# Kernel optimization log

Hardware: AMD Instinct MI355X
Metric: run time of the kernel (lower is better)

The kernel has to match this reference:

```python
import jax, jax.numpy as jnp
import numpy as np

SHIFT = 1  # shift_direction fixed to +1 (module draws +/-1 at random)


def setup_inputs() -> dict:
    key = jax.random.key(0)
    k1, k2 = jax.random.split(key)
    x = jax.random.normal(k1, (128, 48, 28, 28), dtype=jnp.float32)
    w = jax.random.normal(k2, (24, 96, 7), dtype=jnp.float32)  # (Cin, Cout, K) per group, shared across groups
    return {"x": x, "w": w}


def reference(x, w):
    B, H, W = 128, 28, 28
    G, CIN, COUT, K = 2, 24, 96, 7
    # x -> (B, G, Cin, H, W); the unfold/einsum is a grouped conv1d over W (axis 'm'),
    # with H (axis 'n') untouched -> fold H into the batch dim.
    x5 = x.reshape(B, G, CIN, H, W)
    xc = x5.transpose(0, 3, 1, 2, 4).reshape(B * H, G * CIN, W)  # (B*H, 48, W)
    # kernel (Cout, Cin, K); same weights for both groups -> tile to (G*Cout, Cin, K)
    kern = jnp.tile(jnp.transpose(w, (1, 0, 2)), (G, 1, 1))  # (192, 24, 7)
    y = jax.lax.conv_general_dilated(
        xc, kern, window_strides=(1,), padding=[(3, 3)],
        dimension_numbers=('NCH', 'OIH', 'NCH'), feature_group_count=G)  # (B*H, 192, W)
    y = y.reshape(B, H, G * COUT, W).transpose(0, 2, 1, 3)  # (B, 192, H, W), channels group-major = (o, i)
    return jnp.roll(y, SHIFT, axis=2)  # roll along H (original dim 2)
```

## Files before the change

kernel.cpp:

```cpp
#include <hip/hip_runtime.h>


typedef __attribute__((ext_vector_type(8))) short short8;
typedef __attribute__((ext_vector_type(4))) float float4v;

#define B_     128
#define H_     28
#define W_     28
#define CIN_   24
#define COUT_  96
#define K_     7
#define KSTEPS 6
#define NT_    6
#define MT_    7
#define HW_    784

static __device__ __forceinline__ short f2bf(float f) {
    union { float f; unsigned u; } v; v.f = f;
    return (short)((v.u + 0x7fffu + ((v.u >> 16) & 1u)) >> 16);
}

static __device__ __forceinline__ unsigned cvt_pk_bf16(float a, float b) {
    unsigned r;
    asm("v_cvt_pk_bf16_f32 %0, %1, %2" : "=v"(r) : "v"(a), "v"(b));
    return r;
}

__global__ __launch_bounds__(64)
void wfrag_kernel(const float* __restrict__ w, short8* __restrict__ wf) {
    const int idx  = blockIdx.x;
    const int ks   = idx / 6, nt = idx - ks * 6;
    const int lane = threadIdx.x;
    const int c    = nt * 16 + (lane & 15);
    const int q    = ks * 4 + (lane >> 4);
    short8 v;
    if (q < 21) {
        const int k   = (q * 11) >> 5;
        const int ci0 = (q - 3 * k) * 8;
#pragma unroll
        for (int j = 0; j < 8; ++j)
            v[j] = f2bf(w[(ci0 + j) * (COUT_ * K_) + c * K_ + k]);
    } else {
#pragma unroll
        for (int j = 0; j < 8; ++j) v[j] = 0;
    }
    wf[idx * 64 + lane] = v;
}

__global__ __launch_bounds__(384, 6)
void conv_mfma_kernel(const float* __restrict__ x,
                      const short8* __restrict__ wfg,
                      float* __restrict__ out) {
    const int bid = blockIdx.x;
    const int ht  = bid % 7;
    const int bg  = bid / 7;
    const int g   = bg & 1;
    const int b   = bg >> 1;
    const int tid  = threadIdx.x;
    const int lane = tid & 63;
    const int nt   = tid >> 6;
    const int cgrp = lane & 15;
    const int kgrp = lane >> 4;

    __shared__ __align__(16) short xs[4 * 36 * 24];

    float v0r[5], v1r[5];
#pragma unroll
    for (int it = 0; it < 5; ++it) {
        const int idx = tid + it * 384;
        if (idx < 1728) {
            const int p  = idx % 36;
            const int r  = idx / 36;
            const int cp = r % 12;
            const int hl = r / 12;
            const int ws = p - 3;
            const int rsrc = (4 * ht + hl + 27) % 28;
            float a0 = 0.0f, a1 = 0.0f;
            if (ws >= 0 && ws < W_) {
                const size_t base =
                    ((size_t)(b * 48 + g * CIN_ + cp * 2) * H_ + rsrc) * W_ + ws;
                a0 = x[base];
                a1 = x[base + (size_t)HW_];
            }
            v0r[it] = a0; v1r[it] = a1;
        }
    }

    short8 br[KSTEPS];
#pragma unroll
    for (int ks = 0; ks < KSTEPS; ++ks)
        br[ks] = wfg[(ks * NT_ + nt) * 64 + lane];

#pragma unroll
    for (int it = 0; it < 5; ++it) {
        const int idx = tid + it * 384;
        if (idx < 1728) {
            const int p  = idx % 36;
            const int r  = idx / 36;
            const int cp = r % 12;
            const int hl = r / 12;
            ((unsigned*)xs)[(hl * 36 + p) * 12 + cp] = cvt_pk_bf16(v0r[it], v1r[it]);
        }
    }
    __syncthreads();

    int koff[KSTEPS];
#pragma unroll
    for (int ks = 0; ks < KSTEPS; ++ks) {
        const int q   = ks * 4 + kgrp;
        const int k   = (q * 11) >> 5;
        const int ci0 = (q - 3 * k) * 8;
        koff[ks] = k * 24 + ci0;
    }

    const int c_out = nt * 16 + cgrp;
    float* cbase = out + ((size_t)(b * 192 + g * COUT_ + c_out)) * HW_;

#pragma unroll
    for (int mt = 0; mt < MT_; ++mt) {
        const int mA = mt * 16 + cgrp;
        const int hA = mA / 28;
        const int tA = mA - hA * 28;
        const int abase = (hA * 36 + tA) * 24;
        float4v acc = (float4v)(0.0f);
#pragma unroll
        for (int ks = 0; ks < KSTEPS; ++ks) {
            const short8 a = *(const short8*)&xs[abase + koff[ks]];
            acc = __builtin_amdgcn_mfma_f32_16x16x32_bf16(a, br[ks], acc, 0, 0, 0);
        }
        const int m0 = mt * 16 + kgrp * 4;
        const int hl = m0 / 28;
        const int t0 = m0 - hl * 28;
        const int hd = 4 * ht + hl;
        float4 v; v.x = acc[0]; v.y = acc[1]; v.z = acc[2]; v.w = acc[3];
        *(float4*)&cbase[hd * W_ + t0] = v;
    }
}

extern "C" void kernel_launch(void* const* d_in, const int* in_sizes, int n_in,
                              void* d_out, int out_size, void* d_ws, size_t ws_size,
                              hipStream_t stream) {
    const float* x = (const float*)d_in[0];
    const float* w = (const float*)d_in[1];
    float* out = (float*)d_out;
    short8* wf = (short8*)d_ws;

    wfrag_kernel<<<36, 64, 0, stream>>>(w, wf);
    conv_mfma_kernel<<<B_ * 2 * 7, 384, 0, stream>>>(x, wf, out);
}
```

Baseline: 28.24 us.

## Split waves over M and N-pairs to reuse A fragments; pad LDS rows

Each wave now computes two 16-column output tiles (N-pair) for half of the M tiles instead of one N tile for all seven M tiles, so every LDS A-fragment load feeds two MFMAs. The LDS row stride is padded from 24 to 26 shorts to reduce bank conflicts on the fragment reads. In exchange each wave holds twice the B fragments and two accumulators, raising register pressure, so launch bounds drop occupancy from 6 to 4. The M split is also uneven (4 tiles versus 3), which leaves some waves idle at the end.

```diff
diff --git a/kernel.cpp b/kernel.cpp
--- a/kernel.cpp
+++ b/kernel.cpp
@@ -12,8 +12,8 @@
 #define K_     7
 #define KSTEPS 6
 #define NT_    6
-#define MT_    7
 #define HW_    784
+#define XROW   26
 
 static __device__ __forceinline__ short f2bf(float f) {
     union { float f; unsigned u; } v; v.f = f;
@@ -47,7 +47,7 @@
     wf[idx * 64 + lane] = v;
 }
 
-__global__ __launch_bounds__(384, 6)
+__global__ __launch_bounds__(384, 4)
 void conv_mfma_kernel(const float* __restrict__ x,
                       const short8* __restrict__ wfg,
                       float* __restrict__ out) {
@@ -58,11 +58,13 @@
     const int b   = bg >> 1;
     const int tid  = threadIdx.x;
     const int lane = tid & 63;
-    const int nt   = tid >> 6;
+    const int wv   = tid >> 6;
+    const int np   = wv >> 1;
+    const int mh   = wv & 1;
     const int cgrp = lane & 15;
     const int kgrp = lane >> 4;
 
-    __shared__ __align__(16) short xs[4 * 36 * 24];
+    __shared__ __align__(16) short xs[4 * 36 * XROW];
 
     float v0r[5], v1r[5];
 #pragma unroll
@@ -86,10 +88,12 @@
         }
     }
 
-    short8 br[KSTEPS];
+    short8 br0[KSTEPS], br1[KSTEPS];
 #pragma unroll
-    for (int ks = 0; ks < KSTEPS; ++ks)
-        br[ks] = wfg[(ks * NT_ + nt) * 64 + lane];
+    for (int ks = 0; ks < KSTEPS; ++ks) {
+        br0[ks] = wfg[(ks * NT_ + 2 * np)     * 64 + lane];
+        br1[ks] = wfg[(ks * NT_ + 2 * np + 1) * 64 + lane];
+    }
 
 #pragma unroll
     for (int it = 0; it < 5; ++it) {
@@ -99,7 +103,7 @@
             const int r  = idx / 36;
             const int cp = r % 12;
             const int hl = r / 12;
-            ((unsigned*)xs)[(hl * 36 + p) * 12 + cp] = cvt_pk_bf16(v0r[it], v1r[it]);
+            ((unsigned*)xs)[(hl * 36 + p) * 13 + cp] = cvt_pk_bf16(v0r[it], v1r[it]);
         }
     }
     __syncthreads();
@@ -110,30 +114,42 @@
         const int q   = ks * 4 + kgrp;
         const int k   = (q * 11) >> 5;
         const int ci0 = (q - 3 * k) * 8;
-        koff[ks] = k * 24 + ci0;
+        koff[ks] = k * XROW + ci0;
     }
 
-    const int c_out = nt * 16 + cgrp;
-    float* cbase = out + ((size_t)(b * 192 + g * COUT_ + c_out)) * HW_;
+    const int c_out0 = (2 * np)     * 16 + cgrp;
+    const int c_out1 = (2 * np + 1) * 16 + cgrp;
+    float* cb0 = out + ((size_t)(b * 192 + g * COUT_ + c_out0)) * HW_;
+    float* cb1 = out + ((size_t)(b * 192 + g * COUT_ + c_out1)) * HW_;
+
+    const int mt0 = mh * 4;
+    const int mtn = mh ? 3 : 4;
 
 #pragma unroll
-    for (int mt = 0; mt < MT_; ++mt) {
-        const int mA = mt * 16 + cgrp;
-        const int hA = mA / 28;
-        const int tA = mA - hA * 28;
-        const int abase = (hA * 36 + tA) * 24;
-        float4v acc = (float4v)(0.0f);
+    for (int mti = 0; mti < 4; ++mti) {
+        if (mti < mtn) {
+            const int mt = mt0 + mti;
+            const int mA = mt * 16 + cgrp;
+            const int hA = mA / 28;
+            const int tA = mA - hA * 28;
+            const int abase = (hA * 36 + tA) * XROW;
+            float4v a0 = (float4v)(0.0f);
+            float4v a1 = (float4v)(0.0f);
 #pragma unroll
-        for (int ks = 0; ks < KSTEPS; ++ks) {
-            const short8 a = *(const short8*)&xs[abase + koff[ks]];
-            acc = __builtin_amdgcn_mfma_f32_16x16x32_bf16(a, br[ks], acc, 0, 0, 0);
+            for (int ks = 0; ks < KSTEPS; ++ks) {
+                const short8 a = *(const short8*)&xs[abase + koff[ks]];
+                a0 = __builtin_amdgcn_mfma_f32_16x16x32_bf16(a, br0[ks], a0, 0, 0, 0);
+                a1 = __builtin_amdgcn_mfma_f32_16x16x32_bf16(a, br1[ks], a1, 0, 0, 0);
+            }
+            const int m0 = mt * 16 + kgrp * 4;
+            const int hl = m0 / 28;
+            const int t0 = m0 - hl * 28;
+            const int hd = 4 * ht + hl;
+            float4 u0; u0.x = a0[0]; u0.y = a0[1]; u0.z = a0[2]; u0.w = a0[3];
+            float4 u1; u1.x = a1[0]; u1.y = a1[1]; u1.z = a1[2]; u1.w = a1[3];
+            *(float4*)&cb0[hd * W_ + t0] = u0;
+            *(float4*)&cb1[hd * W_ + t0] = u1;
         }
-        const int m0 = mt * 16 + kgrp * 4;
-        const int hl = m0 / 28;
-        const int t0 = m0 - hl * 28;
-        const int hd = 4 * ht + hl;
-        float4 v; v.x = acc[0]; v.y = acc[1]; v.z = acc[2]; v.w = acc[3];
-        *(float4*)&cbase[hd * W_ + t0] = v;
     }
 }
 
```

Measured after the change: 33.27 us. 17.8% more time.

## Pre-transpose input to padded bf16 layout and stream tiles via global_load_lds

Applied to the files above, without the earlier changes.

Adds a separate pass that converts x to a padded, rolled, channel-pair-packed bf16 buffer in workspace, with the weight-fragment build folded into that same pass. The conv kernel then copies its contiguous slice straight into LDS with global_load_lds, which removes the per-thread strided gather, the conversion and the register staging. In exchange the whole input is written to and read back from global memory in an extra kernel. The old path is kept as a fallback when the workspace is too small.

```diff
diff --git a/kernel.cpp b/kernel.cpp
--- a/kernel.cpp
+++ b/kernel.cpp
@@ -14,25 +14,32 @@
 #define NT_    6
 #define MT_    7
 #define HW_    784
+#define WFBYTES   36864
+#define XBFDWORDS 3096576
+#define XBFBYTES  (XBFDWORDS * 4)
 
 static __device__ __forceinline__ short f2bf(float f) {
     union { float f; unsigned u; } v; v.f = f;
     return (short)((v.u + 0x7fffu + ((v.u >> 16) & 1u)) >> 16);
 }
-
 static __device__ __forceinline__ unsigned cvt_pk_bf16(float a, float b) {
     unsigned r;
     asm("v_cvt_pk_bf16_f32 %0, %1, %2" : "=v"(r) : "v"(a), "v"(b));
     return r;
 }
 
-__global__ __launch_bounds__(64)
-void wfrag_kernel(const float* __restrict__ w, short8* __restrict__ wf) {
-    const int idx  = blockIdx.x;
-    const int ks   = idx / 6, nt = idx - ks * 6;
-    const int lane = threadIdx.x;
-    const int c    = nt * 16 + (lane & 15);
-    const int q    = ks * 4 + (lane >> 4);
+static __device__ __forceinline__ void gload_lds16(const void* g, void* l) {
+    __builtin_amdgcn_global_load_lds(
+        (const __attribute__((address_space(1))) unsigned*)g,
+        (__attribute__((address_space(3))) unsigned*)l, 16, 0, 0);
+}
+
+static __device__ __forceinline__ void wfrag_build(const float* __restrict__ w,
+                                                   short8* __restrict__ wf,
+                                                   int idx, int lane) {
+    const int ks = idx / 6, nt = idx - ks * 6;
+    const int c  = nt * 16 + (lane & 15);
+    const int q  = ks * 4 + (lane >> 4);
     short8 v;
     if (q < 21) {
         const int k   = (q * 11) >> 5;
@@ -47,10 +54,103 @@
     wf[idx * 64 + lane] = v;
 }
 
+__global__ __launch_bounds__(256)
+void xpose_kernel(const float* __restrict__ x, unsigned* __restrict__ xbf,
+                  const float* __restrict__ w, short8* __restrict__ wf) {
+    const int i  = blockIdx.x * 256 + threadIdx.x;
+    const int cp = i % 12;
+    const int r1 = i / 12;
+    const int p  = r1 % 36;
+    const int r2 = r1 / 36;
+    const int hd = r2 % 28;
+    const int bg = r2 / 28;
+    const int g  = bg & 1;
+    const int b  = bg >> 1;
+    const int rsrc = hd ? hd - 1 : 27;
+    const int ws = p - 3;
+    float v0 = 0.0f, v1 = 0.0f;
+    if (ws >= 0 && ws < W_) {
+        const size_t base = ((size_t)(b * 48 + g * CIN_ + 2 * cp) * H_ + rsrc) * W_ + ws;
+        v0 = x[base];
+        v1 = x[base + (size_t)HW_];
+    }
+    xbf[i] = cvt_pk_bf16(v0, v1);
+
+    if (blockIdx.x < 36 && threadIdx.x < 64)
+        wfrag_build(w, wf, blockIdx.x, threadIdx.x);
+}
+
 __global__ __launch_bounds__(384, 6)
-void conv_mfma_kernel(const float* __restrict__ x,
+void conv_mfma_kernel(const unsigned* __restrict__ xbf,
                       const short8* __restrict__ wfg,
                       float* __restrict__ out) {
+    const int bid = blockIdx.x;
+    const int ht  = bid % 7;
+    const int bg  = bid / 7;
+    const int g   = bg & 1;
+    const int b   = bg >> 1;
+    const int tid  = threadIdx.x;
+    const int lane = tid & 63;
+    const int nt   = tid >> 6;
+    const int cgrp = lane & 15;
+    const int kgrp = lane >> 4;
+
+    __shared__ __align__(16) short xs[4 * 36 * 24];
+
+    const char* slice = (const char*)xbf + (size_t)(bg * 28 + 4 * ht) * 1728;
+    gload_lds16(slice + nt * 1024 + lane * 16, (char*)xs + nt * 1024);
+    if (nt == 0 && lane < 48)
+        gload_lds16(slice + 6144 + lane * 16, (char*)xs + 6144);
+
+    short8 br[KSTEPS];
+#pragma unroll
+    for (int ks = 0; ks < KSTEPS; ++ks)
+        br[ks] = wfg[(ks * NT_ + nt) * 64 + lane];
+
+    __syncthreads();
+
+    int koff[KSTEPS];
+#pragma unroll
+    for (int ks = 0; ks < KSTEPS; ++ks) {
+        const int q   = ks * 4 + kgrp;
+        const int k   = (q * 11) >> 5;
+        const int ci0 = (q - 3 * k) * 8;
+        koff[ks] = k * 24 + ci0;
+    }
+
+    const int c_out = nt * 16 + cgrp;
+    float* cbase = out + ((size_t)(b * 192 + g * COUT_ + c_out)) * HW_;
+
+#pragma unroll
+    for (int mt = 0; mt < MT_; ++mt) {
+        const int mA = mt * 16 + cgrp;
+        const int hA = mA / 28;
+        const int tA = mA - hA * 28;
+        const int abase = (hA * 36 + tA) * 24;
+        float4v acc = (float4v)(0.0f);
+#pragma unroll
+        for (int ks = 0; ks < KSTEPS; ++ks) {
+            const short8 a = *(const short8*)&xs[abase + koff[ks]];
+            acc = __builtin_amdgcn_mfma_f32_16x16x32_bf16(a, br[ks], acc, 0, 0, 0);
+        }
+        const int m0 = mt * 16 + kgrp * 4;
+        const int hl = m0 / 28;
+        const int t0 = m0 - hl * 28;
+        const int hd = 4 * ht + hl;
+        float4 v; v.x = acc[0]; v.y = acc[1]; v.z = acc[2]; v.w = acc[3];
+        *(float4*)&cbase[hd * W_ + t0] = v;
+    }
+}
+
+__global__ __launch_bounds__(64)
+void wfrag_kernel(const float* __restrict__ w, short8* __restrict__ wf) {
+    wfrag_build(w, wf, blockIdx.x, threadIdx.x);
+}
+
+__global__ __launch_bounds__(384, 6)
+void conv_fallback_kernel(const float* __restrict__ x,
+                          const short8* __restrict__ wfg,
+                          float* __restrict__ out) {
     const int bid = blockIdx.x;
     const int ht  = bid % 7;
     const int bg  = bid / 7;
@@ -85,12 +185,10 @@
             v0r[it] = a0; v1r[it] = a1;
         }
     }
-
     short8 br[KSTEPS];
 #pragma unroll
     for (int ks = 0; ks < KSTEPS; ++ks)
         br[ks] = wfg[(ks * NT_ + nt) * 64 + lane];
-
 #pragma unroll
     for (int it = 0; it < 5; ++it) {
         const int idx = tid + it * 384;
@@ -112,10 +210,8 @@
         const int ci0 = (q - 3 * k) * 8;
         koff[ks] = k * 24 + ci0;
     }
-
     const int c_out = nt * 16 + cgrp;
     float* cbase = out + ((size_t)(b * 192 + g * COUT_ + c_out)) * HW_;
-
 #pragma unroll
     for (int mt = 0; mt < MT_; ++mt) {
         const int mA = mt * 16 + cgrp;
@@ -143,8 +239,14 @@
     const float* x = (const float*)d_in[0];
     const float* w = (const float*)d_in[1];
     float* out = (float*)d_out;
-    short8* wf = (short8*)d_ws;
-
-    wfrag_kernel<<<36, 64, 0, stream>>>(w, wf);
-    conv_mfma_kernel<<<B_ * 2 * 7, 384, 0, stream>>>(x, wf, out);
-}
+    short8*   wf  = (short8*)d_ws;
+    unsigned* xbf = (unsigned*)((char*)d_ws + WFBYTES);
+
+    if (ws_size >= (size_t)WFBYTES + XBFBYTES) {
+        xpose_kernel<<<XBFDWORDS / 256, 256, 0, stream>>>(x, xbf, w, wf);
+        conv_mfma_kernel<<<B_ * 2 * 7, 384, 0, stream>>>(xbf, wf, out);
+    } else {
+        wfrag_kernel<<<36, 64, 0, stream>>>(w, wf);
+        conv_fallback_kernel<<<B_ * 2 * 7, 384, 0, stream>>>(x, wf, out);
+    }
+}
```

Result: slower. 36.75 us (+30.1%).

## Process a whole image per block instead of four-row tiles

Applied to the files above, without the earlier changes.

Each block now loads all 28 rows of one (batch, group) slice into LDS, in four chunks, and runs 49 M-tiles. The grid shrinks seven-fold and the occupancy hint is dropped. This amortises weight-fragment loads and index overhead per block. In exchange, far fewer blocks and larger LDS per block reduce latency hiding and the overlap of load and compute across blocks.

```diff
diff --git a/kernel.cpp b/kernel.cpp
--- a/kernel.cpp
+++ b/kernel.cpp
@@ -12,14 +12,13 @@
 #define K_     7
 #define KSTEPS 6
 #define NT_    6
-#define MT_    7
 #define HW_    784
+#define NDW    12096
 
 static __device__ __forceinline__ short f2bf(float f) {
     union { float f; unsigned u; } v; v.f = f;
     return (short)((v.u + 0x7fffu + ((v.u >> 16) & 1u)) >> 16);
 }
-
 static __device__ __forceinline__ unsigned cvt_pk_bf16(float a, float b) {
     unsigned r;
     asm("v_cvt_pk_bf16_f32 %0, %1, %2" : "=v"(r) : "v"(a), "v"(b));
@@ -47,13 +46,11 @@
     wf[idx * 64 + lane] = v;
 }
 
-__global__ __launch_bounds__(384, 6)
+__global__ __launch_bounds__(384)
 void conv_mfma_kernel(const float* __restrict__ x,
                       const short8* __restrict__ wfg,
                       float* __restrict__ out) {
-    const int bid = blockIdx.x;
-    const int ht  = bid % 7;
-    const int bg  = bid / 7;
+    const int bg  = blockIdx.x;
     const int g   = bg & 1;
     const int b   = bg >> 1;
     const int tid  = threadIdx.x;
@@ -62,44 +59,45 @@
     const int cgrp = lane & 15;
     const int kgrp = lane >> 4;
 
-    __shared__ __align__(16) short xs[4 * 36 * 24];
-
-    float v0r[5], v1r[5];
-#pragma unroll
-    for (int it = 0; it < 5; ++it) {
-        const int idx = tid + it * 384;
-        if (idx < 1728) {
-            const int p  = idx % 36;
-            const int r  = idx / 36;
-            const int cp = r % 12;
-            const int hl = r / 12;
-            const int ws = p - 3;
-            const int rsrc = (4 * ht + hl + 27) % 28;
-            float a0 = 0.0f, a1 = 0.0f;
-            if (ws >= 0 && ws < W_) {
-                const size_t base =
-                    ((size_t)(b * 48 + g * CIN_ + cp * 2) * H_ + rsrc) * W_ + ws;
-                a0 = x[base];
-                a1 = x[base + (size_t)HW_];
-            }
-            v0r[it] = a0; v1r[it] = a1;
-        }
-    }
+    __shared__ __align__(16) short xs[28 * 36 * 24];
 
     short8 br[KSTEPS];
 #pragma unroll
     for (int ks = 0; ks < KSTEPS; ++ks)
         br[ks] = wfg[(ks * NT_ + nt) * 64 + lane];
 
+    for (int ch = 0; ch < 4; ++ch) {
+        float v0r[8], v1r[8];
 #pragma unroll
-    for (int it = 0; it < 5; ++it) {
-        const int idx = tid + it * 384;
-        if (idx < 1728) {
-            const int p  = idx % 36;
-            const int r  = idx / 36;
-            const int cp = r % 12;
-            const int hl = r / 12;
-            ((unsigned*)xs)[(hl * 36 + p) * 12 + cp] = cvt_pk_bf16(v0r[it], v1r[it]);
+        for (int it = 0; it < 8; ++it) {
+            const int idx = tid + (ch * 8 + it) * 384;
+            if (idx < NDW) {
+                const int p  = idx % 36;
+                const int r  = idx / 36;
+                const int cp = r % 12;
+                const int h  = r / 12;
+                const int ws = p - 3;
+                const int rsrc = h ? h - 1 : 27;
+                float a0 = 0.0f, a1 = 0.0f;
+                if (ws >= 0 && ws < W_) {
+                    const size_t base =
+                        ((size_t)(b * 48 + g * CIN_ + cp * 2) * H_ + rsrc) * W_ + ws;
+                    a0 = x[base];
+                    a1 = x[base + (size_t)HW_];
+                }
+                v0r[it] = a0; v1r[it] = a1;
+            }
+        }
+#pragma unroll
+        for (int it = 0; it < 8; ++it) {
+            const int idx = tid + (ch * 8 + it) * 384;
+            if (idx < NDW) {
+                const int p  = idx % 36;
+                const int r  = idx / 36;
+                const int cp = r % 12;
+                const int h  = r / 12;
+                ((unsigned*)xs)[(h * 36 + p) * 12 + cp] = cvt_pk_bf16(v0r[it], v1r[it]);
+            }
         }
     }
     __syncthreads();
@@ -116,8 +114,8 @@
     const int c_out = nt * 16 + cgrp;
     float* cbase = out + ((size_t)(b * 192 + g * COUT_ + c_out)) * HW_;
 
-#pragma unroll
-    for (int mt = 0; mt < MT_; ++mt) {
+#pragma unroll 7
+    for (int mt = 0; mt < 49; ++mt) {
         const int mA = mt * 16 + cgrp;
         const int hA = mA / 28;
         const int tA = mA - hA * 28;
@@ -128,12 +126,8 @@
             const short8 a = *(const short8*)&xs[abase + koff[ks]];
             acc = __builtin_amdgcn_mfma_f32_16x16x32_bf16(a, br[ks], acc, 0, 0, 0);
         }
-        const int m0 = mt * 16 + kgrp * 4;
-        const int hl = m0 / 28;
-        const int t0 = m0 - hl * 28;
-        const int hd = 4 * ht + hl;
         float4 v; v.x = acc[0]; v.y = acc[1]; v.z = acc[2]; v.w = acc[3];
-        *(float4*)&cbase[hd * W_ + t0] = v;
+        *(float4*)&cbase[mt * 16 + kgrp * 4] = v;
     }
 }
 
@@ -146,5 +140,5 @@
     short8* wf = (short8*)d_ws;
 
     wfrag_kernel<<<36, 64, 0, stream>>>(w, wf);
-    conv_mfma_kernel<<<B_ * 2 * 7, 384, 0, stream>>>(x, wf, out);
+    conv_mfma_kernel<<<B_ * 2, 384, 0, stream>>>(x, wf, out);
 }
```

Result: slower. 30.32 us (+7.4%).
